# Kernel tuning notes

Measured on AMD Instinct MI355X. Metric: run time of the kernel, lower is better.

Reference implementation:

```python
import jax, jax.numpy as jnp
import numpy as np

B = 65536
SEM, COL, LAT, K, NL = 768, 64, 64, 256, 3
EPS_LN = 1e-5

def layernorm(x, g, b):
    m = jnp.mean(x, axis=-1, keepdims=True)
    v = jnp.mean((x - m) ** 2, axis=-1, keepdims=True)
    return (x - m) * jax.lax.rsqrt(v + EPS_LN) * g + b

def l2norm(x):
    n = jnp.sqrt(jnp.sum(x * x, axis=-1, keepdims=True))
    return x / jnp.maximum(n, 1e-12)

def setup_inputs() -> dict:
    key = jax.random.key(0)
    ks = jax.random.split(key, 32)
    g = lambda i, shape, s=0.02: jax.random.normal(ks[i], shape, jnp.float32) * s
    inp = {
        'semantic_emb': jax.random.normal(ks[0], (B, SEM), jnp.float32),
        'collab_emb':   jax.random.normal(ks[1], (B, COL), jnp.float32),
        # gate network: Linear(64,128)+LN+ReLU+Linear(128,64)+Sigmoid
        'gate_w1': g(2, (COL, 128)), 'gate_b1': jnp.zeros((128,)),
        'gate_ln_g': jnp.ones((128,)), 'gate_ln_b': jnp.zeros((128,)),
        'gate_w2': g(3, (128, COL)), 'gate_b2': jnp.zeros((COL,)),
        # fusion layernorm over 832
        'fusion_ln_g': jnp.ones((SEM + COL,)), 'fusion_ln_b': jnp.zeros((SEM + COL,)),
        # encoder (no bias): 832->512->256->128->64, SiLU between
        'enc_w1': g(4, (SEM + COL, 512)), 'enc_w2': g(5, (512, 256)),
        'enc_w3': g(6, (256, 128)),       'enc_w4': g(7, (128, LAT)),
        # shared decoder (no bias): 64->128->256->512, SiLU after each
        'dec_w1': g(8, (LAT, 128)), 'dec_w2': g(9, (128, 256)), 'dec_w3': g(10, (256, 512)),
        # semantic head: 512->1536 (+LN,ReLU) ->768
        'sem_w1': g(11, (512, 2 * SEM)), 'sem_b1': jnp.zeros((2 * SEM,)),
        'sem_ln_g': jnp.ones((2 * SEM,)), 'sem_ln_b': jnp.zeros((2 * SEM,)),
        'sem_w2': g(12, (2 * SEM, SEM)), 'sem_b2': jnp.zeros((SEM,)),
        # collab head: 512->256 (+LN,ReLU) ->64
        'col_w1': g(13, (512, 256)), 'col_b1': jnp.zeros((256,)),
        'col_ln_g': jnp.ones((256,)), 'col_ln_b': jnp.zeros((256,)),
        'col_w2': g(14, (256, COL)), 'col_b2': jnp.zeros((COL,)),
        # residual codebooks [n_layers, n_embed, latent_dim]
        'codebooks': jax.random.normal(ks[15], (NL, K, LAT), jnp.float32),
    }
    return inp

def _forward(semantic_emb, collab_emb, gate_w1, gate_b1, gate_ln_g, gate_ln_b,
             gate_w2, gate_b2, fusion_ln_g, fusion_ln_b,
             enc_w1, enc_w2, enc_w3, enc_w4, dec_w1, dec_w2, dec_w3,
             sem_w1, sem_b1, sem_ln_g, sem_ln_b, sem_w2, sem_b2,
             col_w1, col_b1, col_ln_g, col_ln_b, col_w2, col_b2, codebooks):
    # --- gated fusion (dropout inactive at eval) ---
    h = jax.nn.relu(layernorm(collab_emb @ gate_w1 + gate_b1, gate_ln_g, gate_ln_b))
    gate_values = jax.nn.sigmoid(h @ gate_w2 + gate_b2)
    denoised_collab = gate_values * collab_emb
    fused = layernorm(jnp.concatenate([semantic_emb, denoised_collab], axis=-1),
                      fusion_ln_g, fusion_ln_b)
    # --- encoder MLP ---
    z = jax.nn.silu(fused @ enc_w1)
    z = jax.nn.silu(z @ enc_w2)
    z = jax.nn.silu(z @ enc_w3)
    z = z @ enc_w4  # [B, LAT]
    # --- residual quantization (eval: nearest-neighbor, straight-through) ---
    residual = z
    z_q_total = jnp.zeros_like(z)
    cb_loss = jnp.float32(0.0)
    cm_loss = jnp.float32(0.0)
    codes_list = []
    for l in range(NL):
        residual = l2norm(residual)  # normalize_residuals=True
        cb = codebooks[l]  # [K, LAT]
        # argmin ||r - e||^2 == argmax (r.e - 0.5||e||^2)
        score = residual @ cb.T - 0.5 * jnp.sum(cb * cb, axis=-1)
        codes = jnp.argmax(score, axis=-1)  # [B]
        e = cb[codes]  # [B, LAT]
        cb_loss = cb_loss + jnp.mean((e - jax.lax.stop_gradient(residual)) ** 2)
        cm_loss = cm_loss + jnp.mean((jax.lax.stop_gradient(e) - residual) ** 2)
        z_q_layer = residual + jax.lax.stop_gradient(e - residual)  # straight-through
        z_q_total = z_q_total + z_q_layer
        residual = residual - z_q_layer
        codes_list.append(codes)
    codes = jnp.stack(codes_list, axis=1)  # [B, NL]
    # --- dual decoders ---
    s = jax.nn.silu(z_q_total @ dec_w1)
    s = jax.nn.silu(s @ dec_w2)
    s = jax.nn.silu(s @ dec_w3)  # [B, 512]
    sh = jax.nn.relu(layernorm(s @ sem_w1 + sem_b1, sem_ln_g, sem_ln_b))
    semantic_recon = sh @ sem_w2 + sem_b2
    ch = jax.nn.relu(layernorm(s @ col_w1 + col_b1, col_ln_g, col_ln_b))
    collab_recon = ch @ col_w2 + col_b2
    return semantic_recon, collab_recon, z_q_total, codes, cb_loss, cm_loss, gate_values

def reference(semantic_emb, collab_emb, gate_w1, gate_b1, gate_ln_g, gate_ln_b,
              gate_w2, gate_b2, fusion_ln_g, fusion_ln_b,
              enc_w1, enc_w2, enc_w3, enc_w4, dec_w1, dec_w2, dec_w3,
              sem_w1, sem_b1, sem_ln_g, sem_ln_b, sem_w2, sem_b2,
              col_w1, col_b1, col_ln_g, col_ln_b, col_w2, col_b2, codebooks):
    return _forward(semantic_emb, collab_emb, gate_w1, gate_b1, gate_ln_g, gate_ln_b,
                    gate_w2, gate_b2, fusion_ln_g, fusion_ln_b,
                    enc_w1, enc_w2, enc_w3, enc_w4, dec_w1, dec_w2, dec_w3,
                    sem_w1, sem_b1, sem_ln_g, sem_ln_b, sem_w2, sem_b2,
                    col_w1, col_b1, col_ln_g, col_ln_b, col_w2, col_b2, codebooks)
```

## Files before the change

### kernel.cpp

```cpp
#include <hip/hip_runtime.h>
#include <hip/hip_bf16.h>
#include <math.h>

typedef __bf16 bf16;
typedef __attribute__((ext_vector_type(8))) __bf16 v8bf;
typedef __attribute__((ext_vector_type(4))) float v4f;
typedef _Float16 f16;
typedef __attribute__((ext_vector_type(8))) _Float16 v8h;
typedef __attribute__((ext_vector_type(4))) _Float16 v4h;

__device__ __forceinline__ void xcd_swizzle(int& bm, int& bn) {
  const int nx = gridDim.x;
  const int id = blockIdx.y * nx + blockIdx.x;
  const int slot = id >> 3;
  const int row_in = slot / nx;
  const int bmi = (id & 7) * (gridDim.y >> 3) + row_in;
  const int bni = slot - row_in * nx;
  bm = bmi << 7; bn = bni << 7;
}

__device__ __forceinline__ void xcd_swizzle256(int& bm, int& bn) {
  const int nx = gridDim.x;
  const int id = blockIdx.y * nx + blockIdx.x;
  const int slot = id >> 3;
// ... 201 lines not shown
#pragma unroll
        for (int j = 0; j < 4; ++j) cacc[i][j] = fmaf(a[i], b[j], cacc[i][j]);
    }
#pragma unroll
    for (int i = 0; i < 8; ++i)
#pragma unroll
      for (int j = 0; j < 4; ++j) acc[i][j] += cacc[i][j];
  }

  const int colb = tx * 4;
  if (EPI == 0) {
#pragma unroll
    for (int i = 0; i < 8; ++i) {
      int row = bm + ty * 8 + i;
      float ss = 0.0f;
#pragma unroll
      for (int j = 0; j < 4; ++j) ss += acc[i][j] * acc[i][j];
      ss += __shfl_xor(ss, 1); ss += __shfl_xor(ss, 2); ss += __shfl_xor(ss, 4); ss += __shfl_xor(ss, 8);
      float nrm = fmaxf(sqrtf(ss), 1e-12f);
      *(float4*)(C + (size_t)row * 64 + colb) =
          make_float4(acc[i][0] / nrm, acc[i][1] / nrm, acc[i][2] / nrm, acc[i][3] / nrm);
    }
  } else if (EPI == 1) {
    float bb[4];
#pragma unroll
    for (int j = 0; j < 4; ++j) bb[j] = bias[colb + j];
#pragma unroll
    for (int i = 0; i < 8; ++i) {
      int row = bm + ty * 8 + i;
      *(float4*)(C + (size_t)row * 64 + colb) =
          make_float4(acc[i][0] + bb[0], acc[i][1] + bb[1], acc[i][2] + bb[2], acc[i][3] + bb[3]);
    }
  } else {
    float bb[4];
#pragma unroll
    for (int j = 0; j < 4; ++j) bb[j] = bias[colb + j];
#pragma unroll
    for (int i = 0; i < 8; ++i) {
      int row = bm + ty * 8 + i;
      float4 av = *(const float4*)(aux + (size_t)row * 64 + colb);
      float g[4];
#pragma unroll
      for (int j = 0; j < 4; ++j) g[j] = 1.0f / (1.0f + expf(-(acc[i][j] + bb[j])));
      *(float4*)(C + (size_t)row * 64 + colb) = make_float4(g[0], g[1], g[2], g[3]);
      *(float4*)(C2 + (size_t)row * 64 + colb) =
          make_float4(g[0] * av.x, g[1] * av.y, g[2] * av.z, g[3] * av.w);
    }
  }
}

__global__ __launch_bounds__(256) void fuse_ln(
    const float* __restrict__ sem, const float* __restrict__ den,
    const float* __restrict__ fg, const float* __restrict__ fb,
    float* __restrict__ fused) {
  const int w = threadIdx.x >> 6, l = threadIdx.x & 63;
  float fgv[13], fbv[13];
#pragma unroll
  for (int q = 0; q < 12; ++q) { fgv[q] = fg[q * 64 + l]; fbv[q] = fb[q * 64 + l]; }
  fgv[12] = fg[768 + l]; fbv[12] = fb[768 + l];
  for (int it = 0; it < 4; ++it) {
    int r = (blockIdx.x * 4 + w) * 4 + it;
    float sv[12];
#pragma unroll
    for (int q = 0; q < 12; ++q) sv[q] = sem[(size_t)r * 768 + q * 64 + l];
    float dv = den[(size_t)r * 64 + l];
    float s = dv;
#pragma unroll
    for (int q = 0; q < 12; ++q) s += sv[q];
#pragma unroll
    for (int m = 1; m < 64; m <<= 1) s += __shfl_xor(s, m, 64);
    float mean = s * (1.0f / 832.0f);
    float t0 = dv - mean;
    float ss = t0 * t0;
#pragma unroll
    for (int q = 0; q < 12; ++q) { float t = sv[q] - mean; ss += t * t; }
#pragma unroll
    for (int m = 1; m < 64; m <<= 1) ss += __shfl_xor(ss, m, 64);
    float sc = 1.0f / sqrtf(ss * (1.0f / 832.0f) + 1e-5f);
#pragma unroll
    for (int q = 0; q < 12; ++q)
      fused[(size_t)r * 832 + q * 64 + l] = (sv[q] - mean) * sc * fgv[q] + fbv[q];
    fused[(size_t)r * 832 + 768 + l] = t0 * sc * fgv[12] + fbv[12];
  }
}

template <int LAYER>
__global__ __launch_bounds__(256) void argupd(
    const float* __restrict__ scores, const float* __restrict__ cbl,
    float* __restrict__ rn, float* __restrict__ zq, float* __restrict__ codes,
    float* __restrict__ loss, bf16* __restrict__ zqb) {
  const int w = threadIdx.x >> 6, l = threadIdx.x & 63;
  const int base = (blockIdx.x * 4 + w) * 16;
  float lacc = 0.0f;
  for (int it = 0; it < 16; ++it) {
    int r = base + it;
    float4 s4 = *(const float4*)(scores + (size_t)r * 256 + l * 4);
    float bs = s4.x; int bi = l * 4;
    if (s4.y > bs) { bs = s4.y; bi = l * 4 + 1; }
    if (s4.z > bs) { bs = s4.z; bi = l * 4 + 2; }
    if (s4.w > bs) { bs = s4.w; bi = l * 4 + 3; }
#pragma unroll
    for (int m = 1; m < 64; m <<= 1) {
      float os = __shfl_xor(bs, m, 64);
      int oi = __shfl_xor(bi, m, 64);
      if (os > bs || (os == bs && oi < bi)) { bs = os; bi = oi; }
    }
    float e = cbl[bi * 64 + l];
    float rl = rn[(size_t)r * 64 + l];
    float emr = e - rl;
    float zql = rl + emr;
    lacc += emr * emr;
    if (l == 0) codes[r * 3 + LAYER] = (float)bi;
    if (LAYER == 0) {
      zq[(size_t)r * 64 + l] = zql;
    } else if (LAYER == 1) {
      zq[(size_t)r * 64 + l] += zql;
    } else {
      float tot = zq[(size_t)r * 64 + l] + zql;
      zq[(size_t)r * 64 + l] = tot;
      zqb[(size_t)r * 64 + l] = (bf16)tot;
    }
    if (LAYER < 2) {
      float rnew = rl - zql;
      float ss = rnew * rnew;
#pragma unroll
      for (int m = 1; m < 64; m <<= 1) ss += __shfl_xor(ss, m, 64);
      float nrm = fmaxf(sqrtf(ss), 1e-12f);
      rn[(size_t)r * 64 + l] = rnew / nrm;
    }
  }
#pragma unroll
  for (int m = 1; m < 64; m <<= 1) lacc += __shfl_xor(lacc, m, 64);
  if (l == 0) {
    float v = lacc * (1.0f / 4194304.0f);
    atomicAdd(loss, v);
    atomicAdd(loss + 1, v);
  }
}

typedef __attribute__((address_space(3))) void lds_void_t;
typedef __attribute__((address_space(1))) const void gbl_void_t;
__device__ __forceinline__ void gl_lds16(const void* g, void* l) {
  __builtin_amdgcn_global_load_lds((gbl_void_t*)g, (lds_void_t*)l, 16, 0, 0);
}

__global__ __launch_bounds__(256, 3) void hgemm3(
    const float* __restrict__ A, const f16* __restrict__ W0,
    const f16* __restrict__ W1, float* __restrict__ C, int N, int Kd) {
  __shared__ __align__(16) f16 As0[128 * 32];
  __shared__ __align__(16) f16 As1[128 * 32];
  __shared__ __align__(16) f16 Bs0[128 * 32];
  __shared__ __align__(16) f16 Bs1[128 * 32];
  const int tid = threadIdx.x;
  const int w = tid >> 6, l = tid & 63;
  int bm, bn;
  xcd_swizzle(bm, bn);
  const int wm = (w >> 1) << 6, wn = (w & 1) << 6;

  v4f acc[4][4];
  v4f z4 = {0.0f, 0.0f, 0.0f, 0.0f};
#pragma unroll
  for (int i = 0; i < 4; ++i)
#pragma unroll
    for (int j = 0; j < 4; ++j) acc[i][j] = z4;

  const int srow = (w << 5) + (l >> 2);
  const int skc = (l & 3) << 3;
  const f16* gb0 = W0 + (size_t)(bn + srow) * Kd + skc;
  const f16* gb1 = W1 + (size_t)(bn + srow) * Kd + skc;
  char* lb0 = (char*)Bs0 + (w << 11);
  char* lb1 = (char*)Bs1 + (w << 11);

  for (int k0 = 0; k0 < Kd; k0 += 32) {
    __syncthreads();
    gl_lds16(gb0 + k0, lb0);
    gl_lds16(gb0 + (size_t)16 * Kd + k0, lb0 + 1024);
    gl_lds16(gb1 + k0, lb1);
    gl_lds16(gb1 + (size_t)16 * Kd + k0, lb1 + 1024);
#pragma unroll
    for (int jj = 0; jj < 4; ++jj) {
      int idx = tid + 256 * jj;
      int row = idx >> 3, kq = (idx & 7) << 2;
      float4 v = *(const float4*)(A + (size_t)(bm + row) * Kd + k0 + kq);
      v4h h0, h1;
      float x;
      x = v.x * 256.0f; h0.x = (f16)x; h1.x = (f16)(x - (float)h0.x);
      x = v.y * 256.0f; h0.y = (f16)x; h1.y = (f16)(x - (float)h0.y);
      x = v.z * 256.0f; h0.z = (f16)x; h1.z = (f16)(x - (float)h0.z);
      x = v.w * 256.0f; h0.w = (f16)x; h1.w = (f16)(x - (float)h0.w);
      *(v4h*)(&As0[row * 32 + kq]) = h0;
      *(v4h*)(&As1[row * 32 + kq]) = h1;
    }
    __syncthreads();
    v8h a0f[4], a1f[4], b0f[4], b1f[4];
#pragma unroll
    for (int f = 0; f < 4; ++f) {
      int ro = (wm + f * 16 + (l & 15)) * 32 + ((l >> 4) << 3);
      int co = (wn + f * 16 + (l & 15)) * 32 + ((l >> 4) << 3);
      a0f[f] = *(const v8h*)(As0 + ro);
      a1f[f] = *(const v8h*)(As1 + ro);
      b0f[f] = *(const v8h*)(Bs0 + co);
      b1f[f] = *(const v8h*)(Bs1 + co);
    }
#pragma unroll
    for (int mf = 0; mf < 4; ++mf)
#pragma unroll
      for (int nf = 0; nf < 4; ++nf) {
        acc[mf][nf] = __builtin_amdgcn_mfma_f32_16x16x32_f16(a0f[mf], b1f[nf], acc[mf][nf], 0, 0, 0);
        acc[mf][nf] = __builtin_amdgcn_mfma_f32_16x16x32_f16(a1f[mf], b0f[nf], acc[mf][nf], 0, 0, 0);
        acc[mf][nf] = __builtin_amdgcn_mfma_f32_16x16x32_f16(a0f[mf], b0f[nf], acc[mf][nf], 0, 0, 0);
      }
  }

  const float sc = 1.0f / (256.0f * 2048.0f);
  const int cbase = bn + wn + (l & 15);
#pragma unroll
  for (int mf = 0; mf < 4; ++mf) {
#pragma unroll
    for (int i = 0; i < 4; ++i) {
      int row = bm + wm + mf * 16 + ((l >> 4) << 2) + i;
#pragma unroll
      for (int nf = 0; nf < 4; ++nf) {
        int col = cbase + nf * 16;
        float v = acc[mf][nf][i] * sc;
        v = v / (1.0f + expf(-v));
        C[(size_t)row * N + col] = v;
      }
    }
  }
}

template <int EPI>
__global__ __launch_bounds__(256, 3) void bgemm(
    const bf16* __restrict__ A, const bf16* __restrict__ Wt,
    const float* __restrict__ bias, void* __restrict__ Cv, int N, int Kd) {
  __shared__ __align__(16) bf16 As[128 * 32];
  __shared__ __align__(16) bf16 Bs[128 * 32];
  const int tid = threadIdx.x;
  const int w = tid >> 6, l = tid & 63;
  int bm, bn;
  xcd_swizzle(bm, bn);
  const int wm = (w >> 1) << 6, wn = (w & 1) << 6;

  v4f acc[4][4];
  v4f z4 = {0.0f, 0.0f, 0.0f, 0.0f};
#pragma unroll
  for (int i = 0; i < 4; ++i)
#pragma unroll
    for (int j = 0; j < 4; ++j) acc[i][j] = z4;

  const int srow = (w << 5) + (l >> 2);
  const int skc = (l & 3) << 3;
  const bf16* ga0 = A + (size_t)(bm + srow) * Kd + skc;
  const bf16* gb0 = Wt + (size_t)(bn + srow) * Kd + skc;
  char* la0 = (char*)As + (w << 11);
  char* lb0 = (char*)Bs + (w << 11);

  for (int k0 = 0; k0 < Kd; k0 += 32) {
    __syncthreads();
    gl_lds16(ga0 + k0, la0);
    gl_lds16(ga0 + (size_t)16 * Kd + k0, la0 + 1024);
    gl_lds16(gb0 + k0, lb0);
    gl_lds16(gb0 + (size_t)16 * Kd + k0, lb0 + 1024);
    __syncthreads();
    v8bf af[4], bfr[4];
#pragma unroll
    for (int f = 0; f < 4; ++f) {
      af[f] = *(const v8bf*)(As + (wm + f * 16 + (l & 15)) * 32 + ((l >> 4) << 3));
      bfr[f] = *(const v8bf*)(Bs + (wn + f * 16 + (l & 15)) * 32 + ((l >> 4) << 3));
    }
#pragma unroll
    for (int mf = 0; mf < 4; ++mf)
#pragma unroll
      for (int nf = 0; nf < 4; ++nf)
        acc[mf][nf] = __builtin_amdgcn_mfma_f32_16x16x32_bf16(af[mf], bfr[nf], acc[mf][nf], 0, 0, 0);
  }

  const int cbase = bn + wn + (l & 15);
  float bb[4];
  if (EPI != 0) {
#pragma unroll
    for (int nf = 0; nf < 4; ++nf) bb[nf] = bias[cbase + nf * 16];
  }
#pragma unroll
  for (int mf = 0; mf < 4; ++mf) {
#pragma unroll
    for (int i = 0; i < 4; ++i) {
      int row = bm + wm + mf * 16 + ((l >> 4) << 2) + i;
#pragma unroll
      for (int nf = 0; nf < 4; ++nf) {
        int col = cbase + nf * 16;
        float v = acc[mf][nf][i];
        if (EPI == 0) {
          v = v / (1.0f + __expf(-v));
          ((bf16*)Cv)[(size_t)row * N + col] = (bf16)v;
        } else if (EPI == 1) {
          v += bb[nf];
          ((bf16*)Cv)[(size_t)row * N + col] = (bf16)v;
        } else {
          v += bb[nf];
          ((float*)Cv)[(size_t)row * N + col] = v;
        }
      }
    }
  }
}

__device__ __forceinline__ void stage_half(const bf16* __restrict__ src, int Kd,
                                           int rbase, int k0, char* hb8,
                                           int wid, int l) {
#pragma unroll
  for (int j = 0; j < 2; ++j) {
    int Cc = wid * 128 + j * 64 + l;
    int cc = Cc ^ (((Cc >> 3) & 3) << 1);
    gl_lds16(src + (size_t)(rbase + (cc >> 3)) * Kd + k0 + (cc & 7) * 8,
             hb8 + wid * 2048 + j * 1024);
  }
}

__device__ __forceinline__ v8bf ldsfrag(const char* base, int row, int kb) {
  int p = row * 128 + kb;
  p ^= ((p >> 7) & 3) << 5;
  return *(const v8bf*)(base + p);
}

__device__ __forceinline__ void rd_a(v8bf (&af)[2][4], const char* ab, int mh, int l) {
  const int rb = mh * 64 + (l & 15);
  const int kb = (l >> 4) * 16;
#pragma unroll
  for (int ks = 0; ks < 2; ++ks)
#pragma unroll
    for (int mf = 0; mf < 4; ++mf)
      af[ks][mf] = ldsfrag(ab, rb + mf * 16, ks * 64 + kb);
}

__device__ __forceinline__ void rd_b(v8bf (&bfr)[2][2], const char* bbp, int nh, int wl, int l) {
  const int rb = wl + nh * 32 + (l & 15);
  const int kb = (l >> 4) * 16;
#pragma unroll
  for (int ks = 0; ks < 2; ++ks)
#pragma unroll
    for (int nf = 0; nf < 2; ++nf)
      bfr[ks][nf] = ldsfrag(bbp, rb + nf * 16, ks * 64 + kb);
}

__device__ __forceinline__ void qmfma(v4f (&q)[4][2], const v8bf (&af)[2][4],
                                      const v8bf (&bfr)[2][2]) {
  __builtin_amdgcn_s_setprio(1);
#pragma unroll
  for (int ks = 0; ks < 2; ++ks)
#pragma unroll
    for (int mf = 0; mf < 4; ++mf)
#pragma unroll
      for (int nf = 0; nf < 2; ++nf)
        q[mf][nf] = __builtin_amdgcn_mfma_f32_16x16x32_bf16(af[ks][mf], bfr[ks][nf],
                                                            q[mf][nf], 0, 0, 0);
  __builtin_amdgcn_s_setprio(0);
}

#define PHASE_BAR() do { __builtin_amdgcn_s_barrier(); __builtin_amdgcn_sched_barrier(0); } while (0)
// ... 48 lines not shown
    PHASE_BAR();
    qmfma(acc[0][0], a0, b0);
    PHASE_BAR();
    rd_b(b1, bb, 1, wl, l);
    stage_half(Wt, Kd, bn + 128, kB, stB + 16384, wid, l);
    PHASE_BAR();
    qmfma(acc[0][1], a0, b1);
    PHASE_BAR();
    rd_a(a1, ab, 1, l);
    PHASE_BAR();
    qmfma(acc[1][0], a1, b0);
    PHASE_BAR();
    stage_half(A, Kd, bm, kA, stA, wid, l);
    stage_half(A, Kd, bm + 128, kA, stA + 16384, wid, l);
    PHASE_BAR();
    qmfma(acc[1][1], a1, b1);
    asm volatile("s_waitcnt vmcnt(4)" ::: "memory");
    PHASE_BAR();
  }
  asm volatile("s_waitcnt vmcnt(0)" ::: "memory");

  const int r0 = bm + ha * 128 + ((l >> 4) << 2);
  const int c0 = bn + (wid & 3) * 64 + (l & 15);
  float bb4[2][2];
  if (EPI != 0) {
#pragma unroll
    for (int nh = 0; nh < 2; ++nh)
#pragma unroll
      for (int nf = 0; nf < 2; ++nf) bb4[nh][nf] = bias[c0 + nh * 32 + nf * 16];
  }
#pragma unroll
  for (int mh = 0; mh < 2; ++mh)
#pragma unroll
    for (int mf = 0; mf < 4; ++mf)
#pragma unroll
      for (int i = 0; i < 4; ++i) {
        const int row = r0 + mh * 64 + mf * 16 + i;
#pragma unroll
        for (int nh = 0; nh < 2; ++nh)
#pragma unroll
          for (int nf = 0; nf < 2; ++nf) {
            const int col = c0 + nh * 32 + nf * 16;
            float v = acc[mh][nh][mf][nf][i];
            if (EPI == 0) {
              v = v / (1.0f + __expf(-v));
              ((bf16*)Cv)[(size_t)row * N + col] = (bf16)v;
            } else if (EPI == 1) {
              v += bb4[nh][nf];
              ((bf16*)Cv)[(size_t)row * N + col] = (bf16)v;
            } else {
              v += bb4[nh][nf];
              ((float*)Cv)[(size_t)row * N + col] = v;
            }
          }
      }
}

template <int VPT, typename T>
__global__ __launch_bounds__(256) void ln_relu(T* __restrict__ x,
    const float* __restrict__ g, const float* __restrict__ b) {
  const int N = VPT * 256;
  const size_t base = (size_t)blockIdx.x * N;
  const int tid = threadIdx.x, w = tid >> 6, l = tid & 63;
  float v[VPT];
#pragma unroll
  for (int q = 0; q < VPT; ++q) v[q] = (float)x[base + q * 256 + tid];
  float s = 0.0f;
#pragma unroll
  for (int q = 0; q < VPT; ++q) s += v[q];
#pragma unroll
  for (int m = 1; m < 64; m <<= 1) s += __shfl_xor(s, m, 64);
  __shared__ float red[8];
  if (l == 0) red[w] = s;
  __syncthreads();
  float mean = (red[0] + red[1] + red[2] + red[3]) * (1.0f / N);
  float ss = 0.0f;
#pragma unroll
  for (int q = 0; q < VPT; ++q) { float t = v[q] - mean; ss += t * t; }
#pragma unroll
  for (int m = 1; m < 64; m <<= 1) ss += __shfl_xor(ss, m, 64);
  if (l == 0) red[4 + w] = ss;
  __syncthreads();
  float var = (red[4] + red[5] + red[6] + red[7]) * (1.0f / N);
  float rs = 1.0f / sqrtf(var + 1e-5f);
#pragma unroll
  for (int q = 0; q < VPT; ++q) {
    int j = q * 256 + tid;
    float y = (v[q] - mean) * rs * g[j] + b[j];
    x[base + j] = (T)fmaxf(y, 0.0f);
  }
}

extern "C" void kernel_launch(void* const* d_in, const int* in_sizes, int n_in,
                              void* d_out, int out_size, void* d_ws, size_t ws_size,
                              hipStream_t stream) {
  (void)in_sizes; (void)n_in; (void)out_size; (void)ws_size;
  const float* semI  = (const float*)d_in[0];
  const float* colI  = (const float*)d_in[1];
  const float* gw1   = (const float*)d_in[2];
  const float* gb1   = (const float*)d_in[3];
  const float* glng  = (const float*)d_in[4];
  const float* glnb  = (const float*)d_in[5];
  const float* gw2   = (const float*)d_in[6];
  const float* gb2   = (const float*)d_in[7];
  const float* fg    = (const float*)d_in[8];
  const float* fb    = (const float*)d_in[9];
  const float* ew1   = (const float*)d_in[10];
  const float* ew2   = (const float*)d_in[11];
  const float* ew3   = (const float*)d_in[12];
  const float* ew4   = (const float*)d_in[13];
  const float* dw1   = (const float*)d_in[14];
  const float* dw2   = (const float*)d_in[15];
  const float* dw3   = (const float*)d_in[16];
  const float* sw1   = (const float*)d_in[17];
  const float* sb1   = (const float*)d_in[18];
  const float* slng  = (const float*)d_in[19];
  const float* slnb  = (const float*)d_in[20];
  const float* sw2   = (const float*)d_in[21];
  const float* sb2   = (const float*)d_in[22];
  const float* cw1   = (const float*)d_in[23];
  const float* cb1   = (const float*)d_in[24];
  const float* clng  = (const float*)d_in[25];
  const float* clnb  = (const float*)d_in[26];
  const float* cw2   = (const float*)d_in[27];
  const float* cb2   = (const float*)d_in[28];
  const float* cbk   = (const float*)d_in[29];

  float* out = (float*)d_out;
  char* ws = (char*)d_ws;

  const size_t OUT_SEM = 0, OUT_COL = 50331648, OUT_ZQ = 54525952,
               OUT_CODES = 58720256, OUT_CB = 58916864, OUT_GATE = 58916866;

  bf16* dec1t = (bf16*)(ws + 0);
  bf16* dec2t = (bf16*)(ws + 16384);
  bf16* dec3t = (bf16*)(ws + 81920);
  bf16* sem1t = (bf16*)(ws + 344064);
  bf16* sem2t = (bf16*)(ws + 1916928);
  bf16* col1t = (bf16*)(ws + 4276224);
  float* cbT  = (float*)(ws + 4538368);
  float* nhn  = (float*)(ws + 4734976);
  f16* e1w0   = (f16*)(ws + 4739072);
  f16* e1w1   = (f16*)(ws + 5591040);
  f16* e2w0   = (f16*)(ws + 6443008);
  f16* e2w1   = (f16*)(ws + 6705152);
  f16* e3w0   = (f16*)(ws + 6967296);
  f16* e3w1   = (f16*)(ws + 7032832);
  const size_t WS_A = 8388608, WS_B = 226492416;
  float* fused  = (float*)(ws + WS_A);
  float* scores = (float*)(ws + WS_A);
  bf16*  semh   = (bf16*)(ws + WS_A);
  float* den = (float*)(ws + WS_B);
  float* hn  = (float*)(ws + WS_B + 16777216);
  float* h1  = (float*)(ws + WS_B);
  float* h2  = (float*)(ws + 360710144);
  float* h3  = (float*)(ws + 427819008);
  float* rn  = (float*)(ws + 461373440);
  bf16* zqb  = (bf16*)(ws + WS_B);
  bf16* d1b  = (bf16*)(ws + WS_B + 8388608);
  bf16* d2b  = (bf16*)(ws + WS_B + 25165824);
  bf16* sb   = (bf16*)(ws + WS_B + 58720256);
  float* colh = (float*)(ws + WS_B + 125829120);

  hipMemsetAsync(out + OUT_CB, 0, 2 * sizeof(float), stream);

  wconv_t<<<(64 * 128 + 255) / 256, 256, 0, stream>>>(dw1, dec1t, 64, 128);
  wconv_t<<<(128 * 256 + 255) / 256, 256, 0, stream>>>(dw2, dec2t, 128, 256);
  wconv_t<<<(256 * 512 + 255) / 256, 256, 0, stream>>>(dw3, dec3t, 256, 512);
  wconv_t<<<(512 * 1536 + 255) / 256, 256, 0, stream>>>(sw1, sem1t, 512, 1536);
  wconv_t<<<(1536 * 768 + 255) / 256, 256, 0, stream>>>(sw2, sem2t, 1536, 768);
  wconv_t<<<(512 * 256 + 255) / 256, 256, 0, stream>>>(cw1, col1t, 512, 256);
  wsplit_t<<<(832 * 512 + 255) / 256, 256, 0, stream>>>(ew1, e1w0, e1w1, 832, 512);
  wsplit_t<<<(512 * 256 + 255) / 256, 256, 0, stream>>>(ew2, e2w0, e2w1, 512, 256);
  wsplit_t<<<(256 * 128 + 255) / 256, 256, 0, stream>>>(ew3, e3w0, e3w1, 256, 128);
  cbt_k<<<192, 256, 0, stream>>>(cbk, cbT);
  nhn_k<<<3, 256, 0, stream>>>(cbk, nhn);

  sgemm128<2><<<dim3(1, 512), 256, 0, stream>>>(colI, gw1, gb1, glng, glnb, hn, 128, 64);
  sgemm64<2><<<512, 256, 0, stream>>>(hn, gw2, gb2, colI, out + OUT_GATE, den, 128);
  fuse_ln<<<4096, 256, 0, stream>>>(semI, den, fg, fb, fused);

  hgemm3<<<dim3(4, 512), 256, 0, stream>>>(fused, e1w0, e1w1, h1, 512, 832);
  hgemm3<<<dim3(2, 512), 256, 0, stream>>>(h1, e2w0, e2w1, h2, 256, 512);
  hgemm3<<<dim3(1, 512), 256, 0, stream>>>(h2, e3w0, e3w1, h3, 128, 256);
  sgemm64<0><<<512, 256, 0, stream>>>(h3, ew4, nullptr, nullptr, rn, nullptr, 128);

  sgemm128<1><<<dim3(2, 512), 256, 0, stream>>>(rn, cbT + 0 * 16384, nhn + 0, nullptr, nullptr, scores, 256, 64);
  argupd<0><<<1024, 256, 0, stream>>>(scores, cbk + 0 * 16384, rn, out + OUT_ZQ, out + OUT_CODES, out + OUT_CB, zqb);
  sgemm128<1><<<dim3(2, 512), 256, 0, stream>>>(rn, cbT + 1 * 16384, nhn + 256, nullptr, nullptr, scores, 256, 64);
  argupd<1><<<1024, 256, 0, stream>>>(scores, cbk + 1 * 16384, rn, out + OUT_ZQ, out + OUT_CODES, out + OUT_CB, zqb);
  sgemm128<1><<<dim3(2, 512), 256, 0, stream>>>(rn, cbT + 2 * 16384, nhn + 512, nullptr, nullptr, scores, 256, 64);
  argupd<2><<<1024, 256, 0, stream>>>(scores, cbk + 2 * 16384, rn, out + OUT_ZQ, out + OUT_CODES, out + OUT_CB, zqb);

  bgemm<0><<<dim3(1, 512), 256, 0, stream>>>(zqb, dec1t, nullptr, d1b, 128, 64);
  bgemm8<0><<<dim3(1, 256), 512, 0, stream>>>(d1b, dec2t, nullptr, d2b, 256, 128);
  bgemm8<0><<<dim3(2, 256), 512, 0, stream>>>(d2b, dec3t, nullptr, sb, 512, 256);
  bgemm8<1><<<dim3(6, 256), 512, 0, stream>>>(sb, sem1t, sb1, semh, 1536, 512);
  ln_relu<6, bf16><<<65536, 256, 0, stream>>>(semh, slng, slnb);
  bgemm8<2><<<dim3(3, 256), 512, 0, stream>>>(semh, sem2t, sb2, out + OUT_SEM, 768, 1536);
  bgemm8<2><<<dim3(1, 256), 512, 0, stream>>>(sb, col1t, cb1, colh, 256, 512);
  ln_relu<1, float><<<65536, 256, 0, stream>>>(colh, clng, clnb);
  sgemm64<1><<<512, 256, 0, stream>>>(colh, cw2, cb2, nullptr, out + OUT_COL, nullptr, 256);
}
```

Baseline: 1.941 ms.

## Pre-split encoder activations into fp16 hi/lo planes and pipeline encoder GEMMs

The fused layernorm and the first two encoder GEMM epilogues now write activations directly as two scaled fp16 planes (hi and residual) instead of fp32. This removes the per-tile fp32 load and split conversion from the GEMM mainloop. The first two encoder layers move to a new 256x256-tile, 512-thread kernel that double-buffers LDS with async global-to-LDS loads and interleaves MFMA phases. The third layer uses a simpler variant that loads both A planes straight into LDS. The cost is extra intermediate memory and a larger 128KB LDS footprint per block.

```diff
diff --git a/kernel.cpp b/kernel.cpp
--- a/kernel.cpp
+++ b/kernel.cpp
@@ -277,7 +277,7 @@
 __global__ __launch_bounds__(256) void fuse_ln(
     const float* __restrict__ sem, const float* __restrict__ den,
     const float* __restrict__ fg, const float* __restrict__ fb,
-    float* __restrict__ fused) {
+    f16* __restrict__ fA0, f16* __restrict__ fA1) {
   const int w = threadIdx.x >> 6, l = threadIdx.x & 63;
   float fgv[13], fbv[13];
 #pragma unroll
@@ -303,9 +303,15 @@
     for (int m = 1; m < 64; m <<= 1) ss += __shfl_xor(ss, m, 64);
     float sc = 1.0f / sqrtf(ss * (1.0f / 832.0f) + 1e-5f);
 #pragma unroll
-    for (int q = 0; q < 12; ++q)
-      fused[(size_t)r * 832 + q * 64 + l] = (sv[q] - mean) * sc * fgv[q] + fbv[q];
-    fused[(size_t)r * 832 + 768 + l] = t0 * sc * fgv[12] + fbv[12];
+    for (int q = 0; q < 13; ++q) {
+      float y = (q < 12) ? ((sv[q] - mean) * sc * fgv[q] + fbv[q])
+                         : (t0 * sc * fgv[12] + fbv[12]);
+      float t = y * 256.0f;
+      f16 h0 = (f16)t;
+      size_t idx = (size_t)r * 832 + q * 64 + l;
+      fA0[idx] = h0;
+      fA1[idx] = (f16)(t - (float)h0);
+    }
   }
 }
 
@@ -369,92 +375,6 @@
   __builtin_amdgcn_global_load_lds((gbl_void_t*)g, (lds_void_t*)l, 16, 0, 0);
 }
 
-__global__ __launch_bounds__(256, 3) void hgemm3(
-    const float* __restrict__ A, const f16* __restrict__ W0,
-    const f16* __restrict__ W1, float* __restrict__ C, int N, int Kd) {
-  __shared__ __align__(16) f16 As0[128 * 32];
-  __shared__ __align__(16) f16 As1[128 * 32];
-  __shared__ __align__(16) f16 Bs0[128 * 32];
-  __shared__ __align__(16) f16 Bs1[128 * 32];
-  const int tid = threadIdx.x;
-  const int w = tid >> 6, l = tid & 63;
-  int bm, bn;
-  xcd_swizzle(bm, bn);
-  const int wm = (w >> 1) << 6, wn = (w & 1) << 6;
-
-  v4f acc[4][4];
-  v4f z4 = {0.0f, 0.0f, 0.0f, 0.0f};
-#pragma unroll
-  for (int i = 0; i < 4; ++i)
-#pragma unroll
-    for (int j = 0; j < 4; ++j) acc[i][j] = z4;
-
-  const int srow = (w << 5) + (l >> 2);
-  const int skc = (l & 3) << 3;
-  const f16* gb0 = W0 + (size_t)(bn + srow) * Kd + skc;
-  const f16* gb1 = W1 + (size_t)(bn + srow) * Kd + skc;
-  char* lb0 = (char*)Bs0 + (w << 11);
-  char* lb1 = (char*)Bs1 + (w << 11);
-
-  for (int k0 = 0; k0 < Kd; k0 += 32) {
-    __syncthreads();
-    gl_lds16(gb0 + k0, lb0);
-    gl_lds16(gb0 + (size_t)16 * Kd + k0, lb0 + 1024);
-    gl_lds16(gb1 + k0, lb1);
-    gl_lds16(gb1 + (size_t)16 * Kd + k0, lb1 + 1024);
-#pragma unroll
-    for (int jj = 0; jj < 4; ++jj) {
-      int idx = tid + 256 * jj;
-      int row = idx >> 3, kq = (idx & 7) << 2;
-      float4 v = *(const float4*)(A + (size_t)(bm + row) * Kd + k0 + kq);
-      v4h h0, h1;
-      float x;
-      x = v.x * 256.0f; h0.x = (f16)x; h1.x = (f16)(x - (float)h0.x);
-      x = v.y * 256.0f; h0.y = (f16)x; h1.y = (f16)(x - (float)h0.y);
-      x = v.z * 256.0f; h0.z = (f16)x; h1.z = (f16)(x - (float)h0.z);
-      x = v.w * 256.0f; h0.w = (f16)x; h1.w = (f16)(x - (float)h0.w);
-      *(v4h*)(&As0[row * 32 + kq]) = h0;
-      *(v4h*)(&As1[row * 32 + kq]) = h1;
-    }
-    __syncthreads();
-    v8h a0f[4], a1f[4], b0f[4], b1f[4];
-#pragma unroll
-    for (int f = 0; f < 4; ++f) {
-      int ro = (wm + f * 16 + (l & 15)) * 32 + ((l >> 4) << 3);
-      int co = (wn + f * 16 + (l & 15)) * 32 + ((l >> 4) << 3);
-      a0f[f] = *(const v8h*)(As0 + ro);
-      a1f[f] = *(const v8h*)(As1 + ro);
-      b0f[f] = *(const v8h*)(Bs0 + co);
-      b1f[f] = *(const v8h*)(Bs1 + co);
-    }
-#pragma unroll
-    for (int mf = 0; mf < 4; ++mf)
-#pragma unroll
-      for (int nf = 0; nf < 4; ++nf) {
-        acc[mf][nf] = __builtin_amdgcn_mfma_f32_16x16x32_f16(a0f[mf], b1f[nf], acc[mf][nf], 0, 0, 0);
-        acc[mf][nf] = __builtin_amdgcn_mfma_f32_16x16x32_f16(a1f[mf], b0f[nf], acc[mf][nf], 0, 0, 0);
-        acc[mf][nf] = __builtin_amdgcn_mfma_f32_16x16x32_f16(a0f[mf], b0f[nf], acc[mf][nf], 0, 0, 0);
-      }
-  }
-
-  const float sc = 1.0f / (256.0f * 2048.0f);
-  const int cbase = bn + wn + (l & 15);
-#pragma unroll
-  for (int mf = 0; mf < 4; ++mf) {
-#pragma unroll
-    for (int i = 0; i < 4; ++i) {
-      int row = bm + wm + mf * 16 + ((l >> 4) << 2) + i;
-#pragma unroll
-      for (int nf = 0; nf < 4; ++nf) {
-        int col = cbase + nf * 16;
-        float v = acc[mf][nf][i] * sc;
-        v = v / (1.0f + expf(-v));
-        C[(size_t)row * N + col] = v;
-      }
-    }
-  }
-}
-
 template <int EPI>
 __global__ __launch_bounds__(256, 3) void bgemm(
     const bf16* __restrict__ A, const bf16* __restrict__ Wt,
@@ -531,6 +451,87 @@
   }
 }
 
+__global__ __launch_bounds__(256, 3) void hgemm_p(
+    const f16* __restrict__ A0, const f16* __restrict__ A1,
+    const f16* __restrict__ W0, const f16* __restrict__ W1,
+    float* __restrict__ C, int N, int Kd) {
+  __shared__ __align__(16) f16 As0[128 * 32];
+  __shared__ __align__(16) f16 As1[128 * 32];
+  __shared__ __align__(16) f16 Bs0[128 * 32];
+  __shared__ __align__(16) f16 Bs1[128 * 32];
+  const int tid = threadIdx.x;
+  const int w = tid >> 6, l = tid & 63;
+  int bm, bn;
+  xcd_swizzle(bm, bn);
+  const int wm = (w >> 1) << 6, wn = (w & 1) << 6;
+
+  v4f acc[4][4];
+  v4f z4 = {0.0f, 0.0f, 0.0f, 0.0f};
+#pragma unroll
+  for (int i = 0; i < 4; ++i)
+#pragma unroll
+    for (int j = 0; j < 4; ++j) acc[i][j] = z4;
+
+  const int srow = (w << 5) + (l >> 2);
+  const int skc = (l & 3) << 3;
+  const f16* ga0 = A0 + (size_t)(bm + srow) * Kd + skc;
+  const f16* ga1 = A1 + (size_t)(bm + srow) * Kd + skc;
+  const f16* gb0 = W0 + (size_t)(bn + srow) * Kd + skc;
+  const f16* gb1 = W1 + (size_t)(bn + srow) * Kd + skc;
+  char* la0 = (char*)As0 + (w << 11);
+  char* la1 = (char*)As1 + (w << 11);
+  char* lb0 = (char*)Bs0 + (w << 11);
+  char* lb1 = (char*)Bs1 + (w << 11);
+
+  for (int k0 = 0; k0 < Kd; k0 += 32) {
+    __syncthreads();
+    gl_lds16(ga0 + k0, la0);
+    gl_lds16(ga0 + (size_t)16 * Kd + k0, la0 + 1024);
+    gl_lds16(ga1 + k0, la1);
+    gl_lds16(ga1 + (size_t)16 * Kd + k0, la1 + 1024);
+    gl_lds16(gb0 + k0, lb0);
+    gl_lds16(gb0 + (size_t)16 * Kd + k0, lb0 + 1024);
+    gl_lds16(gb1 + k0, lb1);
+    gl_lds16(gb1 + (size_t)16 * Kd + k0, lb1 + 1024);
+    __syncthreads();
+    v8h a0f[4], a1f[4], b0f[4], b1f[4];
+#pragma unroll
+    for (int f = 0; f < 4; ++f) {
+      int ro = (wm + f * 16 + (l & 15)) * 32 + ((l >> 4) << 3);
+      int co = (wn + f * 16 + (l & 15)) * 32 + ((l >> 4) << 3);
+      a0f[f] = *(const v8h*)(As0 + ro);
+      a1f[f] = *(const v8h*)(As1 + ro);
+      b0f[f] = *(const v8h*)(Bs0 + co);
+      b1f[f] = *(const v8h*)(Bs1 + co);
+    }
+#pragma unroll
+    for (int mf = 0; mf < 4; ++mf)
+#pragma unroll
+      for (int nf = 0; nf < 4; ++nf) {
+        acc[mf][nf] = __builtin_amdgcn_mfma_f32_16x16x32_f16(a0f[mf], b1f[nf], acc[mf][nf], 0, 0, 0);
+        acc[mf][nf] = __builtin_amdgcn_mfma_f32_16x16x32_f16(a1f[mf], b0f[nf], acc[mf][nf], 0, 0, 0);
+        acc[mf][nf] = __builtin_amdgcn_mfma_f32_16x16x32_f16(a0f[mf], b0f[nf], acc[mf][nf], 0, 0, 0);
+      }
+  }
+
+  const float sc = 1.0f / (256.0f * 2048.0f);
+  const int cbase = bn + wn + (l & 15);
+#pragma unroll
+  for (int mf = 0; mf < 4; ++mf) {
+#pragma unroll
+    for (int i = 0; i < 4; ++i) {
+      int row = bm + wm + mf * 16 + ((l >> 4) << 2) + i;
+#pragma unroll
+      for (int nf = 0; nf < 4; ++nf) {
+        int col = cbase + nf * 16;
+        float v = acc[mf][nf][i] * sc;
+        v = v / (1.0f + expf(-v));
+        C[(size_t)row * N + col] = v;
+      }
+    }
+  }
+}
+
 __device__ __forceinline__ void stage_half(const bf16* __restrict__ src, int Kd,
                                            int rbase, int k0, char* hb8,
                                            int wid, int l) {
@@ -685,6 +686,151 @@
               v += bb4[nh][nf];
               ((float*)Cv)[(size_t)row * N + col] = v;
             }
+          }
+      }
+}
+
+__device__ __forceinline__ void stage_plane(const f16* __restrict__ src, int Kd,
+                                            int rbase, int k0, char* base,
+                                            int wid, int l) {
+#pragma unroll
+  for (int j = 0; j < 2; ++j) {
+    int Cc = wid * 128 + j * 64 + l;
+    int cc = Cc ^ ((Cc >> 3) & 3);
+    gl_lds16(src + (size_t)(rbase + (cc >> 2)) * Kd + k0 + (cc & 3) * 8,
+             base + wid * 2048 + j * 1024);
+  }
+}
+
+__device__ __forceinline__ v8h ldsfragh(const char* base, int row, int kb) {
+  int p = row * 64 + kb;
+  p ^= ((p >> 7) & 3) << 4;
+  return *(const v8h*)(base + p);
+}
+
+__device__ __forceinline__ void rd_a3(v8h (&af)[2][4], const char* a0p,
+                                      const char* a1p, int rb, int kb) {
+#pragma unroll
+  for (int mf = 0; mf < 4; ++mf) {
+    af[0][mf] = ldsfragh(a0p, rb + mf * 16, kb);
+    af[1][mf] = ldsfragh(a1p, rb + mf * 16, kb);
+  }
+}
+
+__device__ __forceinline__ void rd_b3(v8h (&bf)[2][2], const char* b0p,
+                                      const char* b1p, int rb, int kb) {
+#pragma unroll
+  for (int nf = 0; nf < 2; ++nf) {
+    bf[0][nf] = ldsfragh(b0p, rb + nf * 16, kb);
+    bf[1][nf] = ldsfragh(b1p, rb + nf * 16, kb);
+  }
+}
+
+__device__ __forceinline__ void qmfma3(v4f (&q)[4][2], const v8h (&af)[2][4],
+                                       const v8h (&bf)[2][2]) {
+  __builtin_amdgcn_s_setprio(1);
+#pragma unroll
+  for (int mf = 0; mf < 4; ++mf)
+#pragma unroll
+    for (int nf = 0; nf < 2; ++nf) {
+      q[mf][nf] = __builtin_amdgcn_mfma_f32_16x16x32_f16(af[0][mf], bf[1][nf], q[mf][nf], 0, 0, 0);
+      q[mf][nf] = __builtin_amdgcn_mfma_f32_16x16x32_f16(af[1][mf], bf[0][nf], q[mf][nf], 0, 0, 0);
+      q[mf][nf] = __builtin_amdgcn_mfma_f32_16x16x32_f16(af[0][mf], bf[0][nf], q[mf][nf], 0, 0, 0);
+    }
+  __builtin_amdgcn_s_setprio(0);
+}
+
+__global__ __launch_bounds__(512, 2) void hgemm38(
+    const f16* __restrict__ A0, const f16* __restrict__ A1,
+    const f16* __restrict__ W0, const f16* __restrict__ W1,
+    f16* __restrict__ O0, f16* __restrict__ O1, int N, int Kd) {
+  __shared__ __align__(16) char smem[131072];
+  const int tid = threadIdx.x;
+  const int wid = tid >> 6, l = tid & 63;
+  int bm, bn;
+  xcd_swizzle256(bm, bn);
+  const int ha = wid >> 2;
+  const int wc = (wid & 3) * 64;
+  const int NT = Kd >> 5;
+  const int kb = (l >> 4) * 16;
+
+  v4f acc[2][2][4][2];
+  v4f z4 = {0.0f, 0.0f, 0.0f, 0.0f};
+#pragma unroll
+  for (int a = 0; a < 2; ++a)
+#pragma unroll
+    for (int b = 0; b < 2; ++b)
+#pragma unroll
+      for (int c = 0; c < 4; ++c)
+#pragma unroll
+        for (int d = 0; d < 2; ++d) acc[a][b][c][d] = z4;
+
+  stage_plane(A0, Kd, bm, 0,  smem + 0,     wid, l);
+  stage_plane(A1, Kd, bm, 0,  smem + 16384, wid, l);
+  stage_plane(W0, Kd, bn, 0,  smem + 32768, wid, l);
+  stage_plane(W1, Kd, bn, 0,  smem + 49152, wid, l);
+  stage_plane(A0, Kd, bm, 32, smem + 65536, wid, l);
+  stage_plane(A1, Kd, bm, 32, smem + 65536 + 16384, wid, l);
+  asm volatile("s_waitcnt vmcnt(4)" ::: "memory");
+  PHASE_BAR();
+
+  for (int K = 0; K < NT; ++K) {
+    const int cur = K & 1;
+    const char* a0p = smem + cur * 65536;
+    const char* a1p = a0p + 16384;
+    const char* b0p = a0p + 32768;
+    const char* b1p = a0p + 49152;
+    char* st = smem + ((K + 1) & 1) * 65536;
+    char* sa = smem + cur * 65536;
+    const int kB = (K + 1 < NT) ? (K + 1) << 5 : 0;
+    const int kA = (K + 2 < NT) ? (K + 2) << 5 : 0;
+    v8h a0[2][4], a1[2][4], b0[2][2], b1[2][2];
+
+    rd_a3(a0, a0p, a1p, ha * 128 + (l & 15), kb);
+    rd_b3(b0, b0p, b1p, wc + (l & 15), kb);
+    stage_plane(W0, Kd, bn, kB, st + 32768, wid, l);
+    PHASE_BAR();
+    qmfma3(acc[0][0], a0, b0);
+    PHASE_BAR();
+    rd_b3(b1, b0p, b1p, wc + 32 + (l & 15), kb);
+    stage_plane(W1, Kd, bn, kB, st + 49152, wid, l);
+    PHASE_BAR();
+    qmfma3(acc[0][1], a0, b1);
+    PHASE_BAR();
+    rd_a3(a1, a0p, a1p, ha * 128 + 64 + (l & 15), kb);
+    PHASE_BAR();
+    qmfma3(acc[1][0], a1, b0);
+    PHASE_BAR();
+    stage_plane(A0, Kd, bm, kA, sa, wid, l);
+    stage_plane(A1, Kd, bm, kA, sa + 16384, wid, l);
+    PHASE_BAR();
+    qmfma3(acc[1][1], a1, b1);
+    asm volatile("s_waitcnt vmcnt(4)" ::: "memory");
+    PHASE_BAR();
+  }
+  asm volatile("s_waitcnt vmcnt(0)" ::: "memory");
+
+  const float sc = 1.0f / (256.0f * 2048.0f);
+  const int r0 = bm + ha * 128 + ((l >> 4) << 2);
+  const int c0 = bn + wc + (l & 15);
+#pragma unroll
+  for (int mh = 0; mh < 2; ++mh)
+#pragma unroll
+    for (int mf = 0; mf < 4; ++mf)
+#pragma unroll
+      for (int i = 0; i < 4; ++i) {
+        const int row = r0 + mh * 64 + mf * 16 + i;
+#pragma unroll
+        for (int nh = 0; nh < 2; ++nh)
+#pragma unroll
+          for (int nf = 0; nf < 2; ++nf) {
+            const int col = c0 + nh * 32 + nf * 16;
+            float v = acc[mh][nh][mf][nf][i] * sc;
+            v = v / (1.0f + expf(-v));
+            float t = v * 256.0f;
+            f16 h0 = (f16)t;
+            O0[(size_t)row * N + col] = h0;
+            O1[(size_t)row * N + col] = (f16)(t - (float)h0);
           }
       }
 }
@@ -780,13 +926,16 @@
   f16* e3w0   = (f16*)(ws + 6967296);
   f16* e3w1   = (f16*)(ws + 7032832);
   const size_t WS_A = 8388608, WS_B = 226492416;
-  float* fused  = (float*)(ws + WS_A);
+  f16* fA0 = (f16*)(ws + WS_A);
+  f16* fA1 = (f16*)(ws + WS_A + 109051904);
   float* scores = (float*)(ws + WS_A);
   bf16*  semh   = (bf16*)(ws + WS_A);
   float* den = (float*)(ws + WS_B);
   float* hn  = (float*)(ws + WS_B + 16777216);
-  float* h1  = (float*)(ws + WS_B);
-  float* h2  = (float*)(ws + 360710144);
+  f16* h1a = (f16*)(ws + WS_B);
+  f16* h1b = (f16*)(ws + WS_B + 67108864);
+  f16* h2a = (f16*)(ws + 360710144);
+  f16* h2b = (f16*)(ws + 360710144 + 33554432);
   float* h3  = (float*)(ws + 427819008);
   float* rn  = (float*)(ws + 461373440);
   bf16* zqb  = (bf16*)(ws + WS_B);
@@ -811,11 +960,11 @@
 
   sgemm128<2><<<dim3(1, 512), 256, 0, stream>>>(colI, gw1, gb1, glng, glnb, hn, 128, 64);
   sgemm64<2><<<512, 256, 0, stream>>>(hn, gw2, gb2, colI, out + OUT_GATE, den, 128);
-  fuse_ln<<<4096, 256, 0, stream>>>(semI, den, fg, fb, fused);
-
-  hgemm3<<<dim3(4, 512), 256, 0, stream>>>(fused, e1w0, e1w1, h1, 512, 832);
-  hgemm3<<<dim3(2, 512), 256, 0, stream>>>(h1, e2w0, e2w1, h2, 256, 512);
-  hgemm3<<<dim3(1, 512), 256, 0, stream>>>(h2, e3w0, e3w1, h3, 128, 256);
+  fuse_ln<<<4096, 256, 0, stream>>>(semI, den, fg, fb, fA0, fA1);
+
+  hgemm38<<<dim3(2, 256), 512, 0, stream>>>(fA0, fA1, e1w0, e1w1, h1a, h1b, 512, 832);
+  hgemm38<<<dim3(1, 256), 512, 0, stream>>>(h1a, h1b, e2w0, e2w1, h2a, h2b, 256, 512);
+  hgemm_p<<<dim3(1, 512), 256, 0, stream>>>(h2a, h2b, e3w0, e3w1, h3, 128, 256);
   sgemm64<0><<<512, 256, 0, stream>>>(h3, ew4, nullptr, nullptr, rn, nullptr, 128);
 
   sgemm128<1><<<dim3(2, 512), 256, 0, stream>>>(rn, cbT + 0 * 16384, nhn + 0, nullptr, nullptr, scores, 256, 64);
```

New measurement: 2.097 ms. 8.1% more time.

## Pre-split encoder activations into f16 hi/lo planes and stage via direct LDS loads

Applied to the files above, without the earlier changes.

The fp32-to-two-f16 split of encoder activations moves out of the GEMM main loop and into the producer epilogues (fuse_ln and the previous encoder GEMM). The new GEMM stages both A planes with global_load_lds into a swizzled LDS layout to avoid bank conflicts. This removes per-tile conversion ALU work and register staging, and the A traffic stays the same size since two f16 planes equal one fp32 array. The cost is extra intermediate buffers and uncoalesced 2-byte scalar stores in the epilogues.

```diff
diff --git a/kernel.cpp b/kernel.cpp
--- a/kernel.cpp
+++ b/kernel.cpp
@@ -277,7 +277,7 @@
 __global__ __launch_bounds__(256) void fuse_ln(
     const float* __restrict__ sem, const float* __restrict__ den,
     const float* __restrict__ fg, const float* __restrict__ fb,
-    float* __restrict__ fused) {
+    f16* __restrict__ fA0, f16* __restrict__ fA1) {
   const int w = threadIdx.x >> 6, l = threadIdx.x & 63;
   float fgv[13], fbv[13];
 #pragma unroll
@@ -303,9 +303,15 @@
     for (int m = 1; m < 64; m <<= 1) ss += __shfl_xor(ss, m, 64);
     float sc = 1.0f / sqrtf(ss * (1.0f / 832.0f) + 1e-5f);
 #pragma unroll
-    for (int q = 0; q < 12; ++q)
-      fused[(size_t)r * 832 + q * 64 + l] = (sv[q] - mean) * sc * fgv[q] + fbv[q];
-    fused[(size_t)r * 832 + 768 + l] = t0 * sc * fgv[12] + fbv[12];
+    for (int q = 0; q < 13; ++q) {
+      float y = (q < 12) ? ((sv[q] - mean) * sc * fgv[q] + fbv[q])
+                         : (t0 * sc * fgv[12] + fbv[12]);
+      float t = y * 256.0f;
+      f16 h0 = (f16)t;
+      size_t idx = (size_t)r * 832 + q * 64 + l;
+      fA0[idx] = h0;
+      fA1[idx] = (f16)(t - (float)h0);
+    }
   }
 }
 
@@ -369,92 +375,6 @@
   __builtin_amdgcn_global_load_lds((gbl_void_t*)g, (lds_void_t*)l, 16, 0, 0);
 }
 
-__global__ __launch_bounds__(256, 3) void hgemm3(
-    const float* __restrict__ A, const f16* __restrict__ W0,
-    const f16* __restrict__ W1, float* __restrict__ C, int N, int Kd) {
-  __shared__ __align__(16) f16 As0[128 * 32];
-  __shared__ __align__(16) f16 As1[128 * 32];
-  __shared__ __align__(16) f16 Bs0[128 * 32];
-  __shared__ __align__(16) f16 Bs1[128 * 32];
-  const int tid = threadIdx.x;
-  const int w = tid >> 6, l = tid & 63;
-  int bm, bn;
-  xcd_swizzle(bm, bn);
-  const int wm = (w >> 1) << 6, wn = (w & 1) << 6;
-
-  v4f acc[4][4];
-  v4f z4 = {0.0f, 0.0f, 0.0f, 0.0f};
-#pragma unroll
-  for (int i = 0; i < 4; ++i)
-#pragma unroll
-    for (int j = 0; j < 4; ++j) acc[i][j] = z4;
-
-  const int srow = (w << 5) + (l >> 2);
-  const int skc = (l & 3) << 3;
-  const f16* gb0 = W0 + (size_t)(bn + srow) * Kd + skc;
-  const f16* gb1 = W1 + (size_t)(bn + srow) * Kd + skc;
-  char* lb0 = (char*)Bs0 + (w << 11);
-  char* lb1 = (char*)Bs1 + (w << 11);
-
-  for (int k0 = 0; k0 < Kd; k0 += 32) {
-    __syncthreads();
-    gl_lds16(gb0 + k0, lb0);
-    gl_lds16(gb0 + (size_t)16 * Kd + k0, lb0 + 1024);
-    gl_lds16(gb1 + k0, lb1);
-    gl_lds16(gb1 + (size_t)16 * Kd + k0, lb1 + 1024);
-#pragma unroll
-    for (int jj = 0; jj < 4; ++jj) {
-      int idx = tid + 256 * jj;
-      int row = idx >> 3, kq = (idx & 7) << 2;
-      float4 v = *(const float4*)(A + (size_t)(bm + row) * Kd + k0 + kq);
-      v4h h0, h1;
-      float x;
-      x = v.x * 256.0f; h0.x = (f16)x; h1.x = (f16)(x - (float)h0.x);
-      x = v.y * 256.0f; h0.y = (f16)x; h1.y = (f16)(x - (float)h0.y);
-      x = v.z * 256.0f; h0.z = (f16)x; h1.z = (f16)(x - (float)h0.z);
-      x = v.w * 256.0f; h0.w = (f16)x; h1.w = (f16)(x - (float)h0.w);
-      *(v4h*)(&As0[row * 32 + kq]) = h0;
-      *(v4h*)(&As1[row * 32 + kq]) = h1;
-    }
-    __syncthreads();
-    v8h a0f[4], a1f[4], b0f[4], b1f[4];
-#pragma unroll
-    for (int f = 0; f < 4; ++f) {
-      int ro = (wm + f * 16 + (l & 15)) * 32 + ((l >> 4) << 3);
-      int co = (wn + f * 16 + (l & 15)) * 32 + ((l >> 4) << 3);
-      a0f[f] = *(const v8h*)(As0 + ro);
-      a1f[f] = *(const v8h*)(As1 + ro);
-      b0f[f] = *(const v8h*)(Bs0 + co);
-      b1f[f] = *(const v8h*)(Bs1 + co);
-    }
-#pragma unroll
-    for (int mf = 0; mf < 4; ++mf)
-#pragma unroll
-      for (int nf = 0; nf < 4; ++nf) {
-        acc[mf][nf] = __builtin_amdgcn_mfma_f32_16x16x32_f16(a0f[mf], b1f[nf], acc[mf][nf], 0, 0, 0);
-        acc[mf][nf] = __builtin_amdgcn_mfma_f32_16x16x32_f16(a1f[mf], b0f[nf], acc[mf][nf], 0, 0, 0);
-        acc[mf][nf] = __builtin_amdgcn_mfma_f32_16x16x32_f16(a0f[mf], b0f[nf], acc[mf][nf], 0, 0, 0);
-      }
-  }
-
-  const float sc = 1.0f / (256.0f * 2048.0f);
-  const int cbase = bn + wn + (l & 15);
-#pragma unroll
-  for (int mf = 0; mf < 4; ++mf) {
-#pragma unroll
-    for (int i = 0; i < 4; ++i) {
-      int row = bm + wm + mf * 16 + ((l >> 4) << 2) + i;
-#pragma unroll
-      for (int nf = 0; nf < 4; ++nf) {
-        int col = cbase + nf * 16;
-        float v = acc[mf][nf][i] * sc;
-        v = v / (1.0f + expf(-v));
-        C[(size_t)row * N + col] = v;
-      }
-    }
-  }
-}
-
 template <int EPI>
 __global__ __launch_bounds__(256, 3) void bgemm(
     const bf16* __restrict__ A, const bf16* __restrict__ Wt,
@@ -525,6 +445,100 @@
         } else {
           v += bb[nf];
           ((float*)Cv)[(size_t)row * N + col] = v;
+        }
+      }
+    }
+  }
+}
+
+__device__ __forceinline__ void stage_plane(const f16* __restrict__ src, int Kd,
+                                            int rbase, int k0, char* base,
+                                            int wid, int l) {
+#pragma unroll
+  for (int j = 0; j < 2; ++j) {
+    int Cc = wid * 128 + j * 64 + l;
+    int cc = Cc ^ ((Cc >> 3) & 3);
+    gl_lds16(src + (size_t)(rbase + (cc >> 2)) * Kd + k0 + (cc & 3) * 8,
+             base + wid * 2048 + j * 1024);
+  }
+}
+
+__device__ __forceinline__ v8h ldsfragh(const char* base, int row, int kb) {
+  int p = row * 64 + kb;
+  p ^= ((p >> 7) & 3) << 4;
+  return *(const v8h*)(base + p);
+}
+
+template <int EPI>
+__global__ __launch_bounds__(256, 3) void hgemmp(
+    const f16* __restrict__ A0, const f16* __restrict__ A1,
+    const f16* __restrict__ W0, const f16* __restrict__ W1,
+    f16* __restrict__ O0, f16* __restrict__ O1, float* __restrict__ Cf,
+    int N, int Kd) {
+  __shared__ __align__(16) char smem[32768];
+  const int tid = threadIdx.x;
+  const int w = tid >> 6, l = tid & 63;
+  int bm, bn;
+  xcd_swizzle(bm, bn);
+  const int wm = (w >> 1) << 6, wn = (w & 1) << 6;
+  const int kb = (l >> 4) << 4;
+
+  char* pa0 = smem;
+  char* pa1 = smem + 8192;
+  char* pb0 = smem + 16384;
+  char* pb1 = smem + 24576;
+
+  v4f acc[4][4];
+  v4f z4 = {0.0f, 0.0f, 0.0f, 0.0f};
+#pragma unroll
+  for (int i = 0; i < 4; ++i)
+#pragma unroll
+    for (int j = 0; j < 4; ++j) acc[i][j] = z4;
+
+  for (int k0 = 0; k0 < Kd; k0 += 32) {
+    __syncthreads();
+    stage_plane(A0, Kd, bm, k0, pa0, w, l);
+    stage_plane(A1, Kd, bm, k0, pa1, w, l);
+    stage_plane(W0, Kd, bn, k0, pb0, w, l);
+    stage_plane(W1, Kd, bn, k0, pb1, w, l);
+    __syncthreads();
+    v8h a0f[4], a1f[4], b0f[4], b1f[4];
+#pragma unroll
+    for (int f = 0; f < 4; ++f) {
+      a0f[f] = ldsfragh(pa0, wm + f * 16 + (l & 15), kb);
+      a1f[f] = ldsfragh(pa1, wm + f * 16 + (l & 15), kb);
+      b0f[f] = ldsfragh(pb0, wn + f * 16 + (l & 15), kb);
+      b1f[f] = ldsfragh(pb1, wn + f * 16 + (l & 15), kb);
+    }
+#pragma unroll
+    for (int mf = 0; mf < 4; ++mf)
+#pragma unroll
+      for (int nf = 0; nf < 4; ++nf) {
+        acc[mf][nf] = __builtin_amdgcn_mfma_f32_16x16x32_f16(a0f[mf], b1f[nf], acc[mf][nf], 0, 0, 0);
+        acc[mf][nf] = __builtin_amdgcn_mfma_f32_16x16x32_f16(a1f[mf], b0f[nf], acc[mf][nf], 0, 0, 0);
+        acc[mf][nf] = __builtin_amdgcn_mfma_f32_16x16x32_f16(a0f[mf], b0f[nf], acc[mf][nf], 0, 0, 0);
+      }
+  }
+
+  const float sc = 1.0f / (256.0f * 2048.0f);
+  const int cbase = bn + wn + (l & 15);
+#pragma unroll
+  for (int mf = 0; mf < 4; ++mf) {
+#pragma unroll
+    for (int i = 0; i < 4; ++i) {
+      int row = bm + wm + mf * 16 + ((l >> 4) << 2) + i;
+#pragma unroll
+      for (int nf = 0; nf < 4; ++nf) {
+        int col = cbase + nf * 16;
+        float v = acc[mf][nf][i] * sc;
+        v = v / (1.0f + expf(-v));
+        if (EPI == 0) {
+          float t = v * 256.0f;
+          f16 h0 = (f16)t;
+          O0[(size_t)row * N + col] = h0;
+          O1[(size_t)row * N + col] = (f16)(t - (float)h0);
+        } else {
+          Cf[(size_t)row * N + col] = v;
         }
       }
     }
@@ -780,13 +794,16 @@
   f16* e3w0   = (f16*)(ws + 6967296);
   f16* e3w1   = (f16*)(ws + 7032832);
   const size_t WS_A = 8388608, WS_B = 226492416;
-  float* fused  = (float*)(ws + WS_A);
+  f16* fA0 = (f16*)(ws + WS_A);
+  f16* fA1 = (f16*)(ws + WS_A + 109051904);
   float* scores = (float*)(ws + WS_A);
   bf16*  semh   = (bf16*)(ws + WS_A);
   float* den = (float*)(ws + WS_B);
   float* hn  = (float*)(ws + WS_B + 16777216);
-  float* h1  = (float*)(ws + WS_B);
-  float* h2  = (float*)(ws + 360710144);
+  f16* h1a = (f16*)(ws + WS_B);
+  f16* h1b = (f16*)(ws + WS_B + 67108864);
+  f16* h2a = (f16*)(ws + 360710144);
+  f16* h2b = (f16*)(ws + 360710144 + 33554432);
   float* h3  = (float*)(ws + 427819008);
   float* rn  = (float*)(ws + 461373440);
   bf16* zqb  = (bf16*)(ws + WS_B);
@@ -811,11 +828,11 @@
 
   sgemm128<2><<<dim3(1, 512), 256, 0, stream>>>(colI, gw1, gb1, glng, glnb, hn, 128, 64);
   sgemm64<2><<<512, 256, 0, stream>>>(hn, gw2, gb2, colI, out + OUT_GATE, den, 128);
-  fuse_ln<<<4096, 256, 0, stream>>>(semI, den, fg, fb, fused);
-
-  hgemm3<<<dim3(4, 512), 256, 0, stream>>>(fused, e1w0, e1w1, h1, 512, 832);
-  hgemm3<<<dim3(2, 512), 256, 0, stream>>>(h1, e2w0, e2w1, h2, 256, 512);
-  hgemm3<<<dim3(1, 512), 256, 0, stream>>>(h2, e3w0, e3w1, h3, 128, 256);
+  fuse_ln<<<4096, 256, 0, stream>>>(semI, den, fg, fb, fA0, fA1);
+
+  hgemmp<0><<<dim3(4, 512), 256, 0, stream>>>(fA0, fA1, e1w0, e1w1, h1a, h1b, nullptr, 512, 832);
+  hgemmp<0><<<dim3(2, 512), 256, 0, stream>>>(h1a, h1b, e2w0, e2w1, h2a, h2b, nullptr, 256, 512);
+  hgemmp<1><<<dim3(1, 512), 256, 0, stream>>>(h2a, h2b, e3w0, e3w1, nullptr, nullptr, h3, 128, 256);
   sgemm64<0><<<512, 256, 0, stream>>>(h3, ew4, nullptr, nullptr, rn, nullptr, 128);
 
   sgemm128<1><<<dim3(2, 512), 256, 0, stream>>>(rn, cbT + 0 * 16384, nhn + 0, nullptr, nullptr, scores, 256, 64);
```

Measured after the change: 1.913 ms. About the same (-1.4%).
